# Optimization experiments

Measured on AMD Instinct MI355X. Metric: run time of the kernel, lower is better.

The kernel has to match this reference:

```python
import jax, jax.numpy as jnp
import numpy as np

N, H, W = 8, 2048, 2048
AH, AW = 64, 64          # fixed action window in CARLE
PAD = (W - AW) // 2      # symmetric zero padding (992) since H, W even
BIRTH = (3,)             # default rule B3/S23 (Conway's Life)
SURVIVE = (2, 3)
MOORE_SHIFTS = [(-1, -1), (-1, 0), (-1, 1),
                (0, -1),           (0, 1),
                (1, -1),  (1, 0),  (1, 1)]


def setup_inputs() -> dict:
    key = jax.random.key(0)
    k1, k2 = jax.random.split(key)
    universe = (jax.random.uniform(k1, (N, 1, H, W)) < 0.15).astype(jnp.float32)
    # sparse toggle action (nonzero so step() applies it, mean<1 so no reset)
    action = (jax.random.uniform(k2, (1, 1, AH, AW)) < 0.05).astype(jnp.float32)
    return {"universe": universe, "action": action}


def _neighbor_count(u):
    # circular-padded 3x3 Moore conv (all-ones kernel, zero center) == sum of 8 rolls
    return sum(jnp.roll(u, s, axis=(2, 3)) for s in MOORE_SHIFTS)


def reference(universe, action):
    # apply_action: crop action window, zero-pad to full grid, XOR into universe.
    # (XOR with an all-zero action is the identity, so applying unconditionally
    # matches step()'s `if torch.sum(action)` branch exactly.)
    a = action[0, 0, :AH, :AW]
    a_full = jnp.pad(a, ((PAD, PAD), (PAD, PAD)))            # [H, W]
    u = jnp.logical_xor(universe.astype(bool), a_full.astype(bool)).astype(jnp.float32)

    nbr = _neighbor_count(u)                                  # [N,1,H,W] counts 0..8
    dead = u == 0.0
    birth_mask = jnp.zeros_like(dead)
    for b in BIRTH:
        birth_mask = birth_mask | (nbr == b)
    survive_mask = jnp.zeros_like(dead)
    for s in SURVIVE:
        survive_mask = survive_mask | (nbr == s)
    nxt = ((dead & birth_mask) | (~dead & survive_mask)).astype(jnp.float32)

    # step(): if mean(action) == 1.0, the universe is reset to all zeros
    reset = jnp.mean(action) == 1.0
    observation = jnp.where(reset, jnp.zeros_like(nxt), nxt)
    return observation
```

## Files before the change

kernel.cpp:

```cpp
#include <hip/hip_runtime.h>

#define NIMG 8
#define H 2048
#define W 2048
#define AH 64
#define AW 64
#define PAD 992
#define CH 16

typedef float f4 __attribute__((ext_vector_type(4)));

__device__ __forceinline__ float rl(float v, int k) {
    return __int_as_float(__builtin_amdgcn_readlane(__float_as_int(v), k));
}

__device__ __forceinline__ f4 load_row(const float* __restrict__ uni,
                                       const float* __restrict__ act,
                                       size_t img, int r, int c) {
    r &= (H - 1);
    f4 v = *reinterpret_cast<const f4*>(uni + img + (size_t)r * W + c);
    if (r >= PAD && r < PAD + AH && c >= PAD && c < PAD + AW) {
        const float* a = act + (r - PAD) * AW + (c - PAD);
        v.x = (v.x != a[0]) ? 1.0f : 0.0f;
        v.y = (v.y != a[1]) ? 1.0f : 0.0f;
        v.z = (v.z != a[2]) ? 1.0f : 0.0f;
        v.w = (v.w != a[3]) ? 1.0f : 0.0f;
    }
    return v;
}

__device__ __forceinline__ f4 make_hs(f4 v, int lane, float hl, float hr) {
    float left  = __shfl_up(v.w, 1);
    float right = __shfl_down(v.x, 1);
    if (lane == 0)  left  = hl;
    if (lane == 63) right = hr;
    f4 hs;
    hs.x = left  + v.x + v.y;
    hs.y = v.x + v.y + v.z;
    hs.z = v.y + v.z + v.w;
    hs.w = v.z + v.w + right;
    return hs;
}

__device__ __forceinline__ f4 life(f4 a, f4 b, f4 c, f4 cen, float keep) {
    f4 nbr3 = a + b + c - cen;
    nbr3.x -= 3.0f; nbr3.y -= 3.0f; nbr3.z -= 3.0f; nbr3.w -= 3.0f;
    f4 o;
    o.x = (__builtin_fabsf(__builtin_fmaf(0.5f, cen.x, nbr3.x)) <= 0.5f) ? keep : 0.0f;
    o.y = (__builtin_fabsf(__builtin_fmaf(0.5f, cen.y, nbr3.y)) <= 0.5f) ? keep : 0.0f;
    o.z = (__builtin_fabsf(__builtin_fmaf(0.5f, cen.z, nbr3.z)) <= 0.5f) ? keep : 0.0f;
    o.w = (__builtin_fabsf(__builtin_fmaf(0.5f, cen.w, nbr3.w)) <= 0.5f) ? keep : 0.0f;
    return o;
}

__global__ __launch_bounds__(256, 8) void carle_life_kernel(
        const float* __restrict__ uni,
        const float* __restrict__ act,
        float* __restrict__ out) {
    __shared__ float red[4];
    const int t    = threadIdx.x;
    const int lane = t & 63;
    const int wvid = t >> 6;

    const int wv  = (blockIdx.x << 2) | wvid;
    const int n   = wv >> 10;
    const int rem = wv & 1023;
    const int sx  = rem & 7;
    const int sy  = rem >> 3;
    const int strip = sx << 8;
    const int y0  = sy * CH;
    const int c   = strip + (lane << 2);
    const size_t img = (size_t)n * (size_t)H * (size_t)W;

    const int hr   = lane & 31;
    const int hcol = (lane < 32) ? ((strip - 1) & (W - 1))
                                 : ((strip + 256) & (W - 1));
    float halo = 0.0f;
    if (hr < CH + 2) {
        const int r = (y0 - 1 + hr) & (H - 1);
        float x = uni[img + (size_t)r * W + hcol];
        if (r >= PAD && r < PAD + AH && hcol >= PAD && hcol < PAD + AW)
            x = (x != act[(r - PAD) * AW + (hcol - PAD)]) ? 1.0f : 0.0f;
        halo = x;
    }

    f4 v0 = load_row(uni, act, img, y0 - 1, c);
    f4 v1 = load_row(uni, act, img, y0,     c);
    f4 v2 = load_row(uni, act, img, y0 + 1, c);
    f4 v3 = load_row(uni, act, img, y0 + 2, c);
    f4 v4 = load_row(uni, act, img, y0 + 3, c);
    f4 v5 = load_row(uni, act, img, y0 + 4, c);

    {
        const f4* a4 = reinterpret_cast<const f4*>(act);
        float s = 0.0f;
        #pragma unroll
        for (int j = 0; j < 4; ++j) {
            f4 a = a4[t * 4 + j];
            s += a.x + a.y + a.z + a.w;
        }
        #pragma unroll
        for (int k = 32; k > 0; k >>= 1) s += __shfl_down(s, k);
        if (lane == 0) red[wvid] = s;
    }
    __syncthreads();
    const float keep =
        ((red[0] + red[1] + red[2] + red[3]) == (float)(AH * AW)) ? 0.0f : 1.0f;

    f4 hsA = make_hs(v0, lane, rl(halo, 0), rl(halo, 32));
    f4 hsB = make_hs(v1, lane, rl(halo, 1), rl(halo, 33));
    f4 cen = v1;

    #pragma unroll
    for (int i = 0; i < CH; i += 2) {
        f4 p0, p1;
        const bool ld0 = (i + 6 < CH + 2);
        const bool ld1 = (i + 7 < CH + 2);
        if (ld0) p0 = load_row(uni, act, img, y0 + i + 5, c);
        if (ld1) p1 = load_row(uni, act, img, y0 + i + 6, c);

        const f4 hsC = make_hs(v2, lane, rl(halo, i + 2), rl(halo, 32 + i + 2));
        const f4 o0  = life(hsA, hsB, hsC, cen, keep);
        __builtin_nontemporal_store(o0,
            reinterpret_cast<f4*>(out + img + (size_t)(y0 + i) * W + c));

        const f4 hsD = make_hs(v3, lane, rl(halo, i + 3), rl(halo, 32 + i + 3));
        const f4 o1  = life(hsB, hsC, hsD, v2, keep);
        __builtin_nontemporal_store(o1,
            reinterpret_cast<f4*>(out + img + (size_t)(y0 + i + 1) * W + c));

        hsA = hsC; hsB = hsD; cen = v3;
        v2 = v4; v3 = v5;
        if (ld0) v4 = p0;
        if (ld1) v5 = p1;
    }
}

extern "C" void kernel_launch(void* const* d_in, const int* in_sizes, int n_in,
                              void* d_out, int out_size, void* d_ws, size_t ws_size,
                              hipStream_t stream) {
    const float* uni = (const float*)d_in[0];
    const float* act = (const float*)d_in[1];
    float* outp = (float*)d_out;
    (void)d_ws;

    carle_life_kernel<<<NIMG * 8 * (H / CH) / 4, 256, 0, stream>>>(uni, act, outp);
}
```

Before: 52.33 us.

## Remap block order across strips and deepen row prefetch pipeline

Blocks are remapped so that consecutive block IDs are spread across the 8 column strips instead of walking a strip contiguously, which changes how memory traffic is distributed across channels. The initial row loads are issued before the halo load, and the register pipeline becomes one row per iteration with seven rows in flight instead of six. The aim is more memory-level parallelism and better DRAM channel spread. It costs more live vector registers and changes locality between neighbouring blocks.

```diff
diff --git a/kernel.cpp b/kernel.cpp
--- a/kernel.cpp
+++ b/kernel.cpp
@@ -62,7 +62,9 @@
     const int lane = t & 63;
     const int wvid = t >> 6;
 
-    const int wv  = (blockIdx.x << 2) | wvid;
+    const int bid = blockIdx.x;
+    const int sb  = ((bid & 7) << 8) | (bid >> 3);
+    const int wv  = (sb << 2) | wvid;
     const int n   = wv >> 10;
     const int rem = wv & 1023;
     const int sx  = rem & 7;
@@ -71,6 +73,14 @@
     const int y0  = sy * CH;
     const int c   = strip + (lane << 2);
     const size_t img = (size_t)n * (size_t)H * (size_t)W;
+
+    f4 vA = load_row(uni, act, img, y0 - 1, c);
+    f4 vB = load_row(uni, act, img, y0,     c);
+    f4 b1 = load_row(uni, act, img, y0 + 1, c);
+    f4 b2 = load_row(uni, act, img, y0 + 2, c);
+    f4 b3 = load_row(uni, act, img, y0 + 3, c);
+    f4 b4 = load_row(uni, act, img, y0 + 4, c);
+    f4 b5 = load_row(uni, act, img, y0 + 5, c);
 
     const int hr   = lane & 31;
     const int hcol = (lane < 32) ? ((strip - 1) & (W - 1))
@@ -83,13 +93,6 @@
             x = (x != act[(r - PAD) * AW + (hcol - PAD)]) ? 1.0f : 0.0f;
         halo = x;
     }
-
-    f4 v0 = load_row(uni, act, img, y0 - 1, c);
-    f4 v1 = load_row(uni, act, img, y0,     c);
-    f4 v2 = load_row(uni, act, img, y0 + 1, c);
-    f4 v3 = load_row(uni, act, img, y0 + 2, c);
-    f4 v4 = load_row(uni, act, img, y0 + 3, c);
-    f4 v5 = load_row(uni, act, img, y0 + 4, c);
 
     {
         const f4* a4 = reinterpret_cast<const f4*>(act);
@@ -107,32 +110,24 @@
     const float keep =
         ((red[0] + red[1] + red[2] + red[3]) == (float)(AH * AW)) ? 0.0f : 1.0f;
 
-    f4 hsA = make_hs(v0, lane, rl(halo, 0), rl(halo, 32));
-    f4 hsB = make_hs(v1, lane, rl(halo, 1), rl(halo, 33));
-    f4 cen = v1;
+    f4 hsA = make_hs(vA, lane, rl(halo, 0), rl(halo, 32));
+    f4 hsB = make_hs(vB, lane, rl(halo, 1), rl(halo, 33));
+    f4 cen = vB;
 
     #pragma unroll
-    for (int i = 0; i < CH; i += 2) {
-        f4 p0, p1;
-        const bool ld0 = (i + 6 < CH + 2);
-        const bool ld1 = (i + 7 < CH + 2);
-        if (ld0) p0 = load_row(uni, act, img, y0 + i + 5, c);
-        if (ld1) p1 = load_row(uni, act, img, y0 + i + 6, c);
+    for (int i = 0; i < CH; ++i) {
+        f4 bn;
+        const bool ld = (i + 7 < CH + 2);
+        if (ld) bn = load_row(uni, act, img, y0 + i + 6, c);
 
-        const f4 hsC = make_hs(v2, lane, rl(halo, i + 2), rl(halo, 32 + i + 2));
-        const f4 o0  = life(hsA, hsB, hsC, cen, keep);
-        __builtin_nontemporal_store(o0,
+        const f4 hsC = make_hs(b1, lane, rl(halo, i + 2), rl(halo, 32 + i + 2));
+        const f4 o   = life(hsA, hsB, hsC, cen, keep);
+        __builtin_nontemporal_store(o,
             reinterpret_cast<f4*>(out + img + (size_t)(y0 + i) * W + c));
 
-        const f4 hsD = make_hs(v3, lane, rl(halo, i + 3), rl(halo, 32 + i + 3));
-        const f4 o1  = life(hsB, hsC, hsD, v2, keep);
-        __builtin_nontemporal_store(o1,
-            reinterpret_cast<f4*>(out + img + (size_t)(y0 + i + 1) * W + c));
-
-        hsA = hsC; hsB = hsD; cen = v3;
-        v2 = v4; v3 = v5;
-        if (ld0) v4 = p0;
-        if (ld1) v5 = p1;
+        hsA = hsB; hsB = hsC; cen = b1;
+        b1 = b2; b2 = b3; b3 = b4; b4 = b5;
+        if (ld) b5 = bn;
     }
 }
 
```

New measurement: 46.91 us, median of 2. 1.12x faster.
